# Optimization experiments

Hardware: AMD Instinct MI355X
Metric: run time of the kernel (lower is better)

## Reference

```python
import jax, jax.numpy as jnp
import numpy as np

WS = 7  # window_size (odd)


def _attn_idx(H, W, ws):
    # replication-pad the arange over the valid (unfolded) grid, matching ReplicationPad2d
    Ho, Wo = H - (ws - 1), W - (ws - 1)
    idx = np.arange(Ho * Wo, dtype=np.int64).reshape(Ho, Wo)
    pad = ws // 2
    idx = np.pad(idx, pad, mode='edge')  # [H, W]
    return jnp.asarray(idx.reshape(-1))  # [H*W]


def _bias_idx(H, W, ws):
    rep_h = np.ones(ws, dtype=np.int64); rep_h[ws // 2] = H - (ws - 1)
    rep_w = np.ones(ws, dtype=np.int64); rep_w[ws // 2] = W - (ws - 1)
    idx_h = np.repeat(np.arange(ws), rep_h)  # [H]
    idx_w = np.repeat(np.arange(ws), rep_w)  # [W]
    bias_hw = idx_h[:, None] * (2 * ws - 1) + idx_w[None, :]  # [H, W]
    idx_k = (np.arange(ws)[:, None] * (2 * ws - 1) + np.arange(ws)).reshape(-1)  # [ws^2]
    bias_idx = bias_hw.reshape(-1)[:, None] + idx_k[None, :]  # [H*W, ws^2]
    return jnp.asarray(bias_idx)


def setup_inputs() -> dict:
    key = jax.random.key(0)
    k0, k1, k2, k3 = jax.random.split(key, 4)
    B, C, H, W = 2, 256, 56, 56
    nh = 8
    x = jax.random.normal(k0, (B, C, H, W), jnp.float32)
    qkv_w = jax.random.normal(k1, (3 * C, C), jnp.float32) * 0.02  # 1x1 conv weight
    qkv_b = jnp.zeros((3 * C,), jnp.float32)
    proj_w = jax.random.normal(k2, (C, C), jnp.float32) * 0.02  # 1x1 conv weight
    proj_b = jnp.zeros((C,), jnp.float32)
    relative_bias = jax.random.normal(k3, ((2 * WS - 1) ** 2, nh), jnp.float32) * 0.02
    return {"x": x, "qkv_w": qkv_w, "qkv_b": qkv_b,
            "proj_w": proj_w, "proj_b": proj_b, "relative_bias": relative_bias}


def reference(x, qkv_w, qkv_b, proj_w, proj_b, relative_bias):
    B, C, H, W = x.shape
    ws = WS
    nh = relative_bias.shape[1]
    hd = C // nh
    scale = hd ** -0.5
    L = (H - ws + 1) * (W - ws + 1)

    # 1x1 conv qkv
    qkv = jnp.einsum('oc,bchw->bohw', qkv_w, x) + qkv_b[None, :, None, None]
    q, k, v = qkv[:, :C], qkv[:, C:2 * C], qkv[:, 2 * C:]
    q = q * scale

    def unfold(t):
        # torch nn.Unfold: [B, C*ws^2, L] with channel-major ordering (c slowest),
        # then .view(B, C, -1, ws^2): row-major reinterpretation (faithful to source)
        p = jax.lax.conv_general_dilated_patches(t, (ws, ws), (1, 1), 'VALID')  # [B,C*ws^2,Ho,Wo]
        return p.reshape(B, C, L, ws * ws)

    attn_idx = _attn_idx(H, W, ws)   # [H*W] indices into L
    bias_idx = _bias_idx(H, W, ws)   # [H*W, ws^2]

    k_u = unfold(k).reshape(B, nh, hd, L, ws * ws).transpose(0, 1, 3, 2, 4)  # [B,nh,L,hd,ws^2]
    v_u = unfold(v).reshape(B, nh, hd, L, ws * ws).transpose(0, 1, 3, 4, 2)  # [B,nh,L,ws^2,hd]
    k_g = k_u[:, :, attn_idx]  # [B,nh,HW,hd,ws^2]
    v_g = v_u[:, :, attn_idx]  # [B,nh,HW,ws^2,hd]

    qh = q.reshape(B, nh, hd, H * W).transpose(0, 1, 3, 2)  # [B,nh,HW,hd]

    attn = jnp.einsum('bnld,bnldk->bnlk', qh, k_g)  # [B,nh,HW,ws^2]
    bias = jnp.transpose(relative_bias[bias_idx], (2, 0, 1))  # [nh,HW,ws^2]
    attn = attn + bias[None]  # NOTE: source applies no softmax; dropout p=0

    out = jnp.einsum('bnlk,bnlkd->bnld', attn, v_g)  # [B,nh,HW,hd]
    out = jnp.transpose(out, (0, 1, 3, 2)).reshape(B, C, H, W)
    out = jnp.einsum('oc,bchw->bohw', proj_w, out) + proj_b[None, :, None, None]
    return out
```

## Files before the change

### kernel.cpp

```cpp
#include <hip/hip_runtime.h>
#include <cstddef>
#include <cstdint>

#define HWT   3136
#define WIMG  56
#define CCH   256
#define NH    8
#define QKV_ELEMS (16 * HWT * 32)
#define SCALE 0.17677669529663687f

typedef __attribute__((ext_vector_type(8))) short short8;
typedef __attribute__((ext_vector_type(4))) short short4v;
typedef __attribute__((ext_vector_type(4))) float f32x4;
typedef _Float16 half2v __attribute__((ext_vector_type(2)));
typedef _Float16 half4v __attribute__((ext_vector_type(4)));

#if defined(__has_builtin)
#if __has_builtin(__builtin_amdgcn_fdot2)
#define HAVE_FDOT2 1
#endif
#endif
#ifndef HAVE_FDOT2
#define HAVE_FDOT2 0
#endif

__device__ __forceinline__ ushort f2bf(float f) {
  union { float f; uint32_t u; } v; v.f = f;
  uint32_t u = v.u;
  u += 0x7fffu + ((u >> 16) & 1u);
  return (ushort)(u >> 16);
}

__global__ __launch_bounds__(256) void prep_k(
    const float* __restrict__ x, const float* __restrict__ qkv_w,
    const float* __restrict__ proj_w, ushort* __restrict__ xt,
    ushort* __restrict__ wq, ushort* __restrict__ wp,
    ushort* __restrict__ src16) {
  if (blockIdx.z == 3) {
    int e = (blockIdx.y * 98 + blockIdx.x) * 256 + threadIdx.x;
    if (e < 2500 * 49) {
      int sp = e / 2500;
      int pos = e - sp * 2500;
      int i = pos / 50 + sp / 7;
      int j = pos % 50 + sp % 7;
      src16[e] = (ushort)(i * WIMG + j);
    }
    return;
  }
  if (blockIdx.z == 2) {
    int base = ((blockIdx.y * 98 + blockIdx.x) * 256 + threadIdx.x) * 2;
#pragma unroll
    for (int e = base; e < base + 2; ++e) {
      if (e < 768 * 256) wq[e] = f2bf(qkv_w[e]);
      else if (e < 768 * 256 + 256 * 256) {
        int e2 = e - 768 * 256;
        wp[e2] = f2bf(proj_w[e2]);
      }
    }
    return;
  }
  __shared__ float tile[32][33];
  const int hw0 = blockIdx.x * 32, c0 = blockIdx.y * 32, b = blockIdx.z;
  const int tx = threadIdx.x & 31, ty = threadIdx.x >> 5;
  const float* xb = x + ((size_t)b * CCH + c0) * HWT + hw0;
#pragma unroll
  for (int i = 0; i < 4; ++i) {
    int c = ty + i * 8;
    tile[c][tx] = xb[(size_t)c * HWT + tx];
  }
  __syncthreads();
  ushort* xo = xt + ((size_t)b * HWT + hw0) * CCH + c0;
#pragma unroll
  for (int i = 0; i < 4; ++i) {
    int hwl = ty + i * 8;
    xo[(size_t)hwl * CCH + tx] = f2bf(tile[tx][hwl]);
  }
}

template <int MODE, int MI>
__global__ __launch_bounds__(256) void mfma_gemm_k(
    const ushort* __restrict__ A, int rowsA,
    const ushort* __restrict__ B, int rowsB,
    const float* __restrict__ biasv, void* __restrict__ outp) {
  __shared__ ushort Alds[MI * 32 * 32];
  __shared__ ushort Blds[128 * 32];

  const int t  = threadIdx.x;
  const int m0 = blockIdx.y * (MI * 32);
  const int n0 = blockIdx.x * 128;
  const int b  = blockIdx.z;

  const ushort* Ab = A;
  const ushort* Bb = B + (size_t)b * HWT * CCH;

  const int lane  = t & 63;
  const int wid   = t >> 6;
  const int wm    = (wid >> 1) * (MI * 16);
  const int wn    = (wid & 1) * 64;
  const int lrow  = lane & 15;
  const int cwant = lane >> 4;
  const int csw   = (cwant ^ ((lrow >> 1) & 3)) * 8;

  const int srow   = t >> 2;
  const int scslot = t & 3;
  const int wlds   = wid << 9;

  f32x4 acc[MI][4];
#pragma unroll
  for (int i = 0; i < MI; ++i)
#pragma unroll
    for (int j = 0; j < 4; ++j) acc[i][j] = (f32x4){0.f, 0.f, 0.f, 0.f};

  for (int k0 = 0; k0 < CCH; k0 += 32) {
    __syncthreads();
#pragma unroll
    for (int h = 0; h < MI / 2; ++h) {
      const int lr   = srow + h * 64;
      const int csrc = (scslot ^ ((lr >> 1) & 3)) * 8;
      int ga = m0 + lr; ga = ga < rowsA ? ga : rowsA - 1;
      const ushort* gpa = Ab + (size_t)ga * CCH + k0 + csrc;
      ushort* lpa = Alds + h * 2048 + wlds;
      __builtin_amdgcn_global_load_lds(
          (const __attribute__((address_space(1))) void*)gpa,
          (__attribute__((address_space(3))) void*)lpa, 16, 0, 0);
    }
#pragma unroll
    for (int h = 0; h < 2; ++h) {
      const int lr   = srow + h * 64;
      const int csrc = (scslot ^ ((lr >> 1) & 3)) * 8;
      int gb = n0 + lr; gb = gb < rowsB ? gb : rowsB - 1;
      const ushort* gpb = Bb + (size_t)gb * CCH + k0 + csrc;
      ushort* lpb = Blds + h * 2048 + wlds;
      __builtin_amdgcn_global_load_lds(
          (const __attribute__((address_space(1))) void*)gpb,
          (__attribute__((address_space(3))) void*)lpb, 16, 0, 0);
    }
    __syncthreads();

    short8 af[MI], bf[4];
#pragma unroll
    for (int mi = 0; mi < MI; ++mi)
      af[mi] = *(const short8*)&Alds[(wm + mi * 16 + lrow) * 32 + csw];
#pragma unroll
    for (int ni = 0; ni < 4; ++ni)
      bf[ni] = *(const short8*)&Blds[(wn + ni * 16 + lrow) * 32 + csw];
#pragma unroll
    for (int mi = 0; mi < MI; ++mi)
#pragma unroll
      for (int ni = 0; ni < 4; ++ni)
        acc[mi][ni] = __builtin_amdgcn_mfma_f32_16x16x32_bf16(
            af[mi], bf[ni], acc[mi][ni], 0, 0, 0);
  }

  const int row4 = (lane >> 4) * 4;
  if (MODE == 0) {
    _Float16* qh = (_Float16*)outp;
#pragma unroll
    for (int mi = 0; mi < MI; ++mi) {
      const int o0 = m0 + wm + mi * 16 + row4;
      const int t3 = o0 >> 8, c0 = o0 & 255;
      const int head = c0 >> 5, d0 = c0 & 31;
      const float sc = (t3 == 0) ? SCALE : 1.f;
      float bv[4];
#pragma unroll
      for (int r = 0; r < 4; ++r) bv[r] = biasv[o0 + r];
      if (t3 == 1) {
        _Float16* base = qh + (size_t)QKV_ELEMS +
                         ((size_t)(b * NH + head) * 4 + (d0 >> 3)) * (HWT * 8) +
                         (d0 & 7);
#pragma unroll
        for (int ni = 0; ni < 4; ++ni) {
          const int hw = n0 + wn + ni * 16 + lrow;
          if (hw < HWT) {
            half4v pack;
#pragma unroll
            for (int r = 0; r < 4; ++r)
              pack[r] = (_Float16)(acc[mi][ni][r] + bv[r]);
            *(half4v*)(base + (size_t)hw * 8) = pack;
          }
        }
      } else {
        _Float16* base = qh + (size_t)t3 * QKV_ELEMS +
                         (size_t)(b * NH + head) * HWT * 32 + d0;
#pragma unroll
        for (int ni = 0; ni < 4; ++ni) {
          const int hw = n0 + wn + ni * 16 + lrow;
          if (hw < HWT) {
            half4v pack;
#pragma unroll
            for (int r = 0; r < 4; ++r)
              pack[r] = (_Float16)((acc[mi][ni][r] + bv[r]) * sc);
            *(half4v*)(base + (size_t)hw * 32) = pack;
          }
        }
      }
    }
  } else {
    float* op = (float*)outp;
#pragma unroll
    for (int mi = 0; mi < MI; ++mi)
#pragma unroll
      for (int r = 0; r < 4; ++r) {
        const int o = m0 + wm + mi * 16 + row4 + r;
        const float bvv = biasv[o];
#pragma unroll
        for (int ni = 0; ni < 4; ++ni) {
          const int hw = n0 + wn + ni * 16 + lrow;
          if (hw < HWT)
            op[((size_t)b * CCH + o) * HWT + hw] = acc[mi][ni][r] + bvv;
        }
      }
  }
}

__global__ __launch_bounds__(256, 4) void attn_v4_k(
    const _Float16* __restrict__ q_h, const _Float16* __restrict__ kt8,
    const _Float16* __restrict__ v_h, const float* __restrict__ relbias,
    const ushort* __restrict__ src16, ushort* __restrict__ att_t) {
  const int id  = blockIdx.x;
  const int idx = (id & 7) * 196 + (id >> 3);
  const int bn  = idx / 98;
  const int g   = idx % 98;
  const int px0 = g * 32;
  const int b = bn >> 3, n = bn & 7;

  __shared__ float bias_s[169];
  __shared__ uint32_t as_lds[32 * 49];

  const int tid = threadIdx.x;
  if (tid < 169) bias_s[tid] = relbias[tid * NH + n];
  __syncthreads();

  const int wid = tid >> 6, lane = tid & 63;
  const int jc = lane < 49 ? lane : 48;
  const int jbias = (jc / 7) * 13 + jc % 7;

  const _Float16* kb = kt8 + (size_t)bn * 4 * HWT * 8;
  const _Float16* vb = v_h + (size_t)bn * HWT * 32;
  const _Float16* qb = q_h + (size_t)bn * HWT * 32;

  const int pxw = px0 + wid * 8;

#pragma unroll
  for (int batch = 0; batch < 4; ++batch) {
    int sv[2], bb[2];
#pragma unroll
    for (int p = 0; p < 2; ++p) {
      const int px = pxw + batch * 2 + p;
      const int h = px / WIMG, w = px % WIMG;
      int ph = h - 3; ph = ph < 0 ? 0 : (ph > 49 ? 49 : ph);
      int pw = w - 3; pw = pw < 0 ? 0 : (pw > 49 ? 49 : pw);
      const int l = ph * 50 + pw;
      const int bih = (h < 3) ? h : ((h < 53) ? 3 : h - 49);
      const int biw = (w < 3) ? w : ((w < 53) ? 3 : w - 49);
      bb[p] = bih * 13 + biw;
      sv[p] = (int)src16[l * 49 + jc];
    }
    union V16 { uint4 u; half2v h2[4]; };
    V16 K[2][4];
#pragma unroll
    for (int p = 0; p < 2; ++p)
#pragma unroll
      for (int dq = 0; dq < 4; ++dq)
        K[p][dq].u = *(const uint4*)(kb + ((size_t)dq * HWT + sv[p]) * 8);

#pragma unroll
    for (int p = 0; p < 2; ++p) {
      const int px = pxw + batch * 2 + p;
      union V64 { uint4 u[4]; half2v hv[16]; };
      V64 Q;
      const uint4* qp = (const uint4*)(qb + (size_t)px * 32);
#pragma unroll
      for (int i = 0; i < 4; ++i) Q.u[i] = qp[i];
      const float bvv = bias_s[bb[p] + jbias];

      float a0 = 0.f, a1 = 0.f, a2 = 0.f, a3 = 0.f;
#if HAVE_FDOT2
#pragma unroll
      for (int i = 0; i < 4; ++i) {
        a0 = __builtin_amdgcn_fdot2(K[p][0].h2[i], Q.hv[i],      a0, false);
        a1 = __builtin_amdgcn_fdot2(K[p][1].h2[i], Q.hv[4 + i],  a1, false);
        a2 = __builtin_amdgcn_fdot2(K[p][2].h2[i], Q.hv[8 + i],  a2, false);
        a3 = __builtin_amdgcn_fdot2(K[p][3].h2[i], Q.hv[12 + i], a3, false);
      }
#else
#pragma unroll
      for (int i = 0; i < 4; ++i) {
        a0 += (float)K[p][0].h2[i][0] * (float)Q.hv[i][0] +
              (float)K[p][0].h2[i][1] * (float)Q.hv[i][1];
        a1 += (float)K[p][1].h2[i][0] * (float)Q.hv[4 + i][0] +
              (float)K[p][1].h2[i][1] * (float)Q.hv[4 + i][1];
        a2 += (float)K[p][2].h2[i][0] * (float)Q.hv[8 + i][0] +
              (float)K[p][2].h2[i][1] * (float)Q.hv[8 + i][1];
        a3 += (float)K[p][3].h2[i][0] * (float)Q.hv[12 + i][0] +
              (float)K[p][3].h2[i][1] * (float)Q.hv[12 + i][1];
      }
#endif
      const float a = (a0 + a1) + (a2 + a3) + bvv;
      union { _Float16 hh; uint16_t us; } cv;
      cv.hh = (_Float16)a;
      if (lane < 49)
        as_lds[(pxw - px0 + batch * 2 + p) * 49 + lane] =
            ((uint32_t)sv[p] << 16) | cv.us;
    }
  }
  __syncthreads();

  const int pxb = tid >> 3, oc = tid & 7;
  const uint32_t* arow = &as_lds[pxb * 49];
  const _Float16* vbase = vb + oc * 4;

  float c0 = 0.f, c1 = 0.f, c2 = 0.f, c3 = 0.f;
#pragma unroll
  for (int gq = 0; gq < 7; ++gq) {
    uint32_t u[7];
#pragma unroll
    for (int i = 0; i < 7; ++i) u[i] = arow[gq * 7 + i];
    half4v vv[7];
#pragma unroll
    for (int i = 0; i < 7; ++i)
      vv[i] = *(const half4v*)(vbase + (size_t)(u[i] >> 16) * 32);
#pragma unroll
    for (int i = 0; i < 7; ++i) {
      union { uint16_t us; _Float16 hh; } cv;
      cv.us = (uint16_t)(u[i] & 0xffffu);
      const float a = (float)cv.hh;
      c0 += a * (float)vv[i][0];
      c1 += a * (float)vv[i][1];
      c2 += a * (float)vv[i][2];
      c3 += a * (float)vv[i][3];
    }
  }

  ushort tmp[4];
  tmp[0] = f2bf(c0); tmp[1] = f2bf(c1);
  tmp[2] = f2bf(c2); tmp[3] = f2bf(c3);
  *(short4v*)(att_t + ((size_t)b * HWT + px0 + pxb) * CCH + n * 32 + oc * 4) =
      *(const short4v*)tmp;
}

extern "C" void kernel_launch(void* const* d_in, const int* in_sizes, int n_in,
                              void* d_out, int out_size, void* d_ws, size_t ws_size,
                              hipStream_t stream) {
  const float* x       = (const float*)d_in[0];
  const float* qkv_w   = (const float*)d_in[1];
  const float* qkv_b   = (const float*)d_in[2];
  const float* proj_w  = (const float*)d_in[3];
  const float* proj_b  = (const float*)d_in[4];
  const float* relbias = (const float*)d_in[5];
  float* out = (float*)d_out;

  char* wsb = (char*)d_ws;
  _Float16* qh  = (_Float16*)wsb;
  _Float16* kt8 = qh + (size_t)QKV_ELEMS;
  _Float16* vh  = qh + (size_t)2 * QKV_ELEMS;
  ushort*   xt  = (ushort*)(wsb + (size_t)3 * QKV_ELEMS * 2);
  ushort*   wq  = xt + (size_t)QKV_ELEMS;
  ushort*   wp  = wq + 768 * 256;
  ushort*   src16 = wp + 256 * 256;
  ushort*   att_t = xt;

  hipLaunchKernelGGL(prep_k, dim3(98, 8, 4), dim3(256), 0, stream,
                     x, qkv_w, proj_w, xt, wq, wp, src16);
  hipLaunchKernelGGL((mfma_gemm_k<0, 4>), dim3(25, 6, 2), dim3(256), 0, stream,
                     wq, 768, xt, HWT, qkv_b, (void*)qh);
  hipLaunchKernelGGL(attn_v4_k, dim3(1568), dim3(256), 0, stream,
                     qh, kt8, vh, relbias, src16, att_t);
  hipLaunchKernelGGL((mfma_gemm_k<1, 2>), dim3(25, 4, 2), dim3(256), 0, stream,
                     wp, 256, att_t, HWT, proj_b, (void*)out);
}
```

Before: 59.54 us.

## Shrink attention blocks to 128 threads, hoist index loads, use packed fp16 AV accumulation

Splits the attention kernel into twice as many 128-thread blocks of 16 pixels each, which gives finer-grained scheduling and a smaller LDS footprint. All eight per-wave gather indices and bias offsets are now loaded up front so those loads can overlap. The query pointer is made wave-uniform with readfirstlane. The attention-times-V accumulation switches from fp32 scalar FMAs to packed half2 multiply-adds over groups of 7, then adds each group into fp32. This raises throughput but costs accuracy, and register use goes up from the hoisted arrays.

```diff
diff --git a/kernel.cpp b/kernel.cpp
--- a/kernel.cpp
+++ b/kernel.cpp
@@ -213,22 +213,22 @@
   }
 }
 
-__global__ __launch_bounds__(256, 4) void attn_v4_k(
+__global__ __launch_bounds__(128, 5) void attn_v5_k(
     const _Float16* __restrict__ q_h, const _Float16* __restrict__ kt8,
     const _Float16* __restrict__ v_h, const float* __restrict__ relbias,
     const ushort* __restrict__ src16, ushort* __restrict__ att_t) {
   const int id  = blockIdx.x;
-  const int idx = (id & 7) * 196 + (id >> 3);
-  const int bn  = idx / 98;
-  const int g   = idx % 98;
-  const int px0 = g * 32;
+  const int idx = (id & 7) * 392 + (id >> 3);
+  const int bn  = idx / 196;
+  const int g   = idx % 196;
+  const int px0 = g * 16;
   const int b = bn >> 3, n = bn & 7;
 
   __shared__ float bias_s[169];
-  __shared__ uint32_t as_lds[32 * 49];
+  __shared__ uint32_t as_lds[16 * 49];
 
   const int tid = threadIdx.x;
-  if (tid < 169) bias_s[tid] = relbias[tid * NH + n];
+  for (int i = tid; i < 169; i += 128) bias_s[i] = relbias[i * NH + n];
   __syncthreads();
 
   const int wid = tid >> 6, lane = tid & 63;
@@ -241,38 +241,41 @@
 
   const int pxw = px0 + wid * 8;
 
+  int sv[8], bb[8];
+#pragma unroll
+  for (int p = 0; p < 8; ++p) {
+    const int px = pxw + p;
+    const int h = px / WIMG, w = px % WIMG;
+    int ph = h - 3; ph = ph < 0 ? 0 : (ph > 49 ? 49 : ph);
+    int pw = w - 3; pw = pw < 0 ? 0 : (pw > 49 ? 49 : pw);
+    const int l = ph * 50 + pw;
+    const int bih = (h < 3) ? h : ((h < 53) ? 3 : h - 49);
+    const int biw = (w < 3) ? w : ((w < 53) ? 3 : w - 49);
+    bb[p] = bih * 13 + biw + jbias;
+    sv[p] = (int)src16[l * 49 + jc];
+  }
+
 #pragma unroll
   for (int batch = 0; batch < 4; ++batch) {
-    int sv[2], bb[2];
-#pragma unroll
-    for (int p = 0; p < 2; ++p) {
-      const int px = pxw + batch * 2 + p;
-      const int h = px / WIMG, w = px % WIMG;
-      int ph = h - 3; ph = ph < 0 ? 0 : (ph > 49 ? 49 : ph);
-      int pw = w - 3; pw = pw < 0 ? 0 : (pw > 49 ? 49 : pw);
-      const int l = ph * 50 + pw;
-      const int bih = (h < 3) ? h : ((h < 53) ? 3 : h - 49);
-      const int biw = (w < 3) ? w : ((w < 53) ? 3 : w - 49);
-      bb[p] = bih * 13 + biw;
-      sv[p] = (int)src16[l * 49 + jc];
-    }
     union V16 { uint4 u; half2v h2[4]; };
     V16 K[2][4];
 #pragma unroll
     for (int p = 0; p < 2; ++p)
 #pragma unroll
       for (int dq = 0; dq < 4; ++dq)
-        K[p][dq].u = *(const uint4*)(kb + ((size_t)dq * HWT + sv[p]) * 8);
+        K[p][dq].u =
+            *(const uint4*)(kb + ((size_t)dq * HWT + sv[batch * 2 + p]) * 8);
 
 #pragma unroll
     for (int p = 0; p < 2; ++p) {
-      const int px = pxw + batch * 2 + p;
+      const int pp = batch * 2 + p;
+      const int pxu = __builtin_amdgcn_readfirstlane(pxw + pp);
       union V64 { uint4 u[4]; half2v hv[16]; };
       V64 Q;
-      const uint4* qp = (const uint4*)(qb + (size_t)px * 32);
+      const uint4* qp = (const uint4*)(qb + (size_t)pxu * 32);
 #pragma unroll
       for (int i = 0; i < 4; ++i) Q.u[i] = qp[i];
-      const float bvv = bias_s[bb[p] + jbias];
+      const float bvv = bias_s[bb[pp]];
 
       float a0 = 0.f, a1 = 0.f, a2 = 0.f, a3 = 0.f;
 #if HAVE_FDOT2
@@ -300,8 +303,7 @@
       union { _Float16 hh; uint16_t us; } cv;
       cv.hh = (_Float16)a;
       if (lane < 49)
-        as_lds[(pxw - px0 + batch * 2 + p) * 49 + lane] =
-            ((uint32_t)sv[p] << 16) | cv.us;
+        as_lds[(wid * 8 + pp) * 49 + lane] = ((uint32_t)sv[pp] << 16) | cv.us;
     }
   }
   __syncthreads();
@@ -310,7 +312,7 @@
   const uint32_t* arow = &as_lds[pxb * 49];
   const _Float16* vbase = vb + oc * 4;
 
-  float c0 = 0.f, c1 = 0.f, c2 = 0.f, c3 = 0.f;
+  float cf0 = 0.f, cf1 = 0.f, cf2 = 0.f, cf3 = 0.f;
 #pragma unroll
   for (int gq = 0; gq < 7; ++gq) {
     uint32_t u[7];
@@ -320,21 +322,25 @@
 #pragma unroll
     for (int i = 0; i < 7; ++i)
       vv[i] = *(const half4v*)(vbase + (size_t)(u[i] >> 16) * 32);
+
+    half2v acc0 = (half2v){(_Float16)0.f, (_Float16)0.f};
+    half2v acc1 = (half2v){(_Float16)0.f, (_Float16)0.f};
 #pragma unroll
     for (int i = 0; i < 7; ++i) {
-      union { uint16_t us; _Float16 hh; } cv;
-      cv.us = (uint16_t)(u[i] & 0xffffu);
-      const float a = (float)cv.hh;
-      c0 += a * (float)vv[i][0];
-      c1 += a * (float)vv[i][1];
-      c2 += a * (float)vv[i][2];
-      c3 += a * (float)vv[i][3];
-    }
+      union { uint32_t w; half2v h; } au;
+      au.w = (u[i] << 16) | (u[i] & 0xffffu);
+      const half2v vlo = (half2v){vv[i][0], vv[i][1]};
+      const half2v vhi = (half2v){vv[i][2], vv[i][3]};
+      acc0 += au.h * vlo;
+      acc1 += au.h * vhi;
+    }
+    cf0 += (float)acc0[0]; cf1 += (float)acc0[1];
+    cf2 += (float)acc1[0]; cf3 += (float)acc1[1];
   }
 
   ushort tmp[4];
-  tmp[0] = f2bf(c0); tmp[1] = f2bf(c1);
-  tmp[2] = f2bf(c2); tmp[3] = f2bf(c3);
+  tmp[0] = f2bf(cf0); tmp[1] = f2bf(cf1);
+  tmp[2] = f2bf(cf2); tmp[3] = f2bf(cf3);
   *(short4v*)(att_t + ((size_t)b * HWT + px0 + pxb) * CCH + n * 32 + oc * 4) =
       *(const short4v*)tmp;
 }
@@ -364,7 +370,7 @@
                      x, qkv_w, proj_w, xt, wq, wp, src16);
   hipLaunchKernelGGL((mfma_gemm_k<0, 4>), dim3(25, 6, 2), dim3(256), 0, stream,
                      wq, 768, xt, HWT, qkv_b, (void*)qh);
-  hipLaunchKernelGGL(attn_v4_k, dim3(1568), dim3(256), 0, stream,
+  hipLaunchKernelGGL(attn_v5_k, dim3(3136), dim3(128), 0, stream,
                      qh, kt8, vh, relbias, src16, att_t);
   hipLaunchKernelGGL((mfma_gemm_k<1, 2>), dim3(25, 4, 2), dim3(256), 0, stream,
                      wp, 256, att_t, HWT, proj_b, (void*)out);
```

New measurement: 54.28 us. 1.1x faster.
